# Optimization experiments

Hardware: AMD Instinct MI355X
Metric: run time of the kernel (lower is better)

## Reference

```python
import jax, jax.numpy as jnp
import numpy as np

HEAD_NUM = 16

def setup_inputs() -> dict:
    key = jax.random.key(0)
    k1, k2, k3, k4, k5 = jax.random.split(key, 5)
    B, S, F = 4, 2048, 1024
    return {
        "X": jax.random.normal(k1, (B, S, F), dtype=jnp.float32),
        "residual_score": jax.random.normal(k2, (B, S, F), dtype=jnp.float32),
        "wq": jax.random.normal(k3, (F, F), dtype=jnp.float32) * 0.05,
        "wk": jax.random.normal(k4, (F, F), dtype=jnp.float32) * 0.05,
        "wv": jax.random.normal(k5, (F, F), dtype=jnp.float32) * 0.05,
    }

def reference(X, residual_score, wq, wk, wv):
    B, S, F = X.shape
    H = HEAD_NUM
    D = F // H  # head dim
    # Original scales logits by sqrt(seq_len / head_num), not sqrt(head_dim).
    scale = jnp.sqrt(jnp.asarray(S / H, dtype=X.dtype))
    # QKV projections: [B,S,F] @ [F,F] -> [B,S,F], then split features into heads -> [B,H,S,D]
    def proj(w):
        y = jnp.einsum('bsf,fg->bsg', X, w)
        return y.reshape(B, S, H, D).transpose(0, 2, 1, 3)
    q, k, v = proj(wq), proj(wk), proj(wv)
    logits = jnp.einsum('bhsd,bhtd->bhst', q, k) / scale  # [B,H,S,S]
    attn = jax.nn.softmax(logits, axis=-1)
    effect = jnp.einsum('bhst,bhtd->bhsd', attn, v)  # [B,H,S,D]
    all_effects = effect.transpose(0, 2, 1, 3).reshape(B, S, F)
    out = all_effects + residual_score
    return (out, out)
```

## Files before the change

### kernel.cpp

```cpp
#include <hip/hip_runtime.h>
#include <hip/hip_bf16.h>
#include <stdint.h>

#define B_ 4
#define S_ 2048
#define F_ 1024
#define H_ 16
#define D_ 64
#define M_ (B_*S_)
#define OUTHALF ((size_t)B_*S_*F_)
#define KVB 64
#define QBLK 256

typedef __attribute__((ext_vector_type(4))) float f32x4;
typedef __attribute__((ext_vector_type(8))) short bf16x8;

__device__ __forceinline__ short f2bf(float f) {
  __hip_bfloat16 h = __float2bfloat16(f);
  return *reinterpret_cast<short*>(&h);
}

__device__ __forceinline__ void gl2lds16(const short* g, short* l) {
  __builtin_amdgcn_global_load_lds(
      (const __attribute__((address_space(1))) uint32_t*)g,
      (__attribute__((address_space(3))) uint32_t*)l, 16, 0, 0);
}

#define VMCNT_BAR(N)                                            \
  do {                                                          \
    asm volatile("s_waitcnt vmcnt(" #N ")" ::: "memory");       \
    __builtin_amdgcn_s_barrier();                               \
    asm volatile("" ::: "memory");                              \
  } while (0)

__global__ __launch_bounds__(256) void convert_x(const float* __restrict__ X,
                                                 short* __restrict__ Xb) {
  int i = (blockIdx.x * 256 + threadIdx.x) * 8;
  f32x4 a = *(const f32x4*)(X + i);
  f32x4 b = *(const f32x4*)(X + i + 4);
  bf16x8 o;
  o[0]=f2bf(a[0]); o[1]=f2bf(a[1]); o[2]=f2bf(a[2]); o[3]=f2bf(a[3]);
  o[4]=f2bf(b[0]); o[5]=f2bf(b[1]); o[6]=f2bf(b[2]); o[7]=f2bf(b[3]);
  *(bf16x8*)(Xb + i) = o;
}

__global__ __launch_bounds__(256) void transpose_w(
    const float* __restrict__ wq, const float* __restrict__ wk, const float* __restrict__ wv,
    short* __restrict__ tq, short* __restrict__ tk, short* __restrict__ tv) {
  const float* W = blockIdx.z == 0 ? wq : (blockIdx.z == 1 ? wk : wv);
  short* T = blockIdx.z == 0 ? tq : (blockIdx.z == 1 ? tk : tv);
  __shared__ float tile[32][33];
  int tx = threadIdx.x, ty = threadIdx.y;
  int x = blockIdx.x * 32 + tx;
  int y0 = blockIdx.y * 32;
  #pragma unroll
  for (int j = ty; j < 32; j += 8) tile[j][tx] = W[(size_t)(y0 + j) * F_ + x];
  __syncthreads();
  int x2 = y0 + tx;
  int y2 = blockIdx.x * 32;
  #pragma unroll
  for (int j = ty; j < 32; j += 8) T[(size_t)(y2 + j) * F_ + x2] = f2bf(tile[tx][j]);
}

__global__ __launch_bounds__(256) void gemm_qkv(
    const short* __restrict__ Xb,
    const short* __restrict__ Wtq, const short* __restrict__ Wtk, const short* __restrict__ Wtv,
    short* __restrict__ Qb, short* __restrict__ Kb, short* __restrict__ Vt) {
  __shared__ short As[2][128 * 32];
  __shared__ short Bs[2][128 * 32];
  const int z = blockIdx.z;
  const short* Wt = z == 0 ? Wtq : (z == 1 ? Wtk : Wtv);
  const int m0 = blockIdx.x * 128, n0 = blockIdx.y * 128;
  const int tid = threadIdx.x, wid = tid >> 6, lane = tid & 63;
  const int wm = wid >> 1, wn = wid & 1;
  const int l15 = lane & 15, l4 = lane >> 4;

  f32x4 acc[4][4];
  #pragma unroll
  for (int i = 0; i < 4; ++i)
    #pragma unroll
    for (int j = 0; j < 4; ++j) acc[i][j] = {0.f, 0.f, 0.f, 0.f};

  const int srow = wid * 32 + (lane >> 2);
  const int scol = (lane & 3) * 8;

  auto stage = [&](int buf, int k0) {
    gl2lds16(Xb + (size_t)(m0 + srow) * F_ + k0 + scol,      &As[buf][(wid * 32) * 32]);
    gl2lds16(Xb + (size_t)(m0 + srow + 16) * F_ + k0 + scol, &As[buf][(wid * 32 + 16) * 32]);
    gl2lds16(Wt + (size_t)(n0 + srow) * F_ + k0 + scol,      &Bs[buf][(wid * 32) * 32]);
    gl2lds16(Wt + (size_t)(n0 + srow + 16) * F_ + k0 + scol, &Bs[buf][(wid * 32 + 16) * 32]);
  };

  stage(0, 0);
  const int NT = F_ / 32;
  for (int t = 0; t < NT; ++t) {
    const int buf = t & 1;
    if (t + 1 < NT) {
      stage(buf ^ 1, (t + 1) * 32);
      VMCNT_BAR(4);
    } else {
      VMCNT_BAR(0);
    }
    bf16x8 a[4], b[4];
    #pragma unroll
    for (int mf = 0; mf < 4; ++mf)
      a[mf] = *(const bf16x8*)&As[buf][(wm * 64 + mf * 16 + l15) * 32 + l4 * 8];
    #pragma unroll
    for (int nf = 0; nf < 4; ++nf)
      b[nf] = *(const bf16x8*)&Bs[buf][(wn * 64 + nf * 16 + l15) * 32 + l4 * 8];
    __builtin_amdgcn_s_setprio(1);
    #pragma unroll
    for (int mf = 0; mf < 4; ++mf)
      #pragma unroll
      for (int nf = 0; nf < 4; ++nf)
        acc[mf][nf] = __builtin_amdgcn_mfma_f32_16x16x32_bf16(a[mf], b[nf], acc[mf][nf], 0, 0, 0);
    __builtin_amdgcn_s_setprio(0);
    __builtin_amdgcn_s_barrier();
    asm volatile("" ::: "memory");
  }

  const float qscale = 0.12751784477559752f;
  #pragma unroll
  for (int mf = 0; mf < 4; ++mf)
    #pragma unroll
    for (int nf = 0; nf < 4; ++nf)
      #pragma unroll
      for (int r = 0; r < 4; ++r) {
        float v = acc[mf][nf][r];
        int row = m0 + wm * 64 + mf * 16 + l4 * 4 + r;
        int col = n0 + wn * 64 + nf * 16 + l15;
        int bb = row >> 11, s = row & 2047, h = col >> 6, d = col & 63;
        if (z == 0)
          Qb[((size_t)(bb * H_ + h) * S_ + s) * D_ + d] = f2bf(v * qscale);
        else if (z == 1)
          Kb[((size_t)(bb * H_ + h) * S_ + s) * D_ + d] = f2bf(v);
        else {
          int s5 = s & 31;
          int sp = (s & ~31) | (((s5 >> 2) & 3) << 3) | (((s5 >> 4) & 1) << 2) | (s5 & 3);
          Vt[((size_t)(bb * H_ + h) * D_ + d) * S_ + sp] = f2bf(v);
        }
      }
}

__global__ __launch_bounds__(512, 4) void attn_kernel(
    const short* __restrict__ Qb, const short* __restrict__ Kb, const short* __restrict__ Vt,
    const float* __restrict__ resid, float* __restrict__ out) {
  __shared__ short Ks[2][KVB][64];
  __shared__ short Vs[2][D_][KVB];
  const int bh = blockIdx.y;
  const int b = bh >> 4, h = bh & 15;
  const int qbase = blockIdx.x * QBLK;
  const int wid = threadIdx.x >> 6, lane = threadIdx.x & 63;
  const int l15 = lane & 15, l4 = lane >> 4;
  const short* Qp = Qb + (size_t)bh * S_ * D_;
  const short* Kp = Kb + (size_t)bh * S_ * D_;
  const short* Vp = Vt + (size_t)bh * D_ * S_;

  bf16x8 bq[2][2];
  #pragma unroll
  for (int g = 0; g < 2; ++g) {
    int qr = qbase + wid * 32 + g * 16 + l15;
    bq[g][0] = *(const bf16x8*)&Qp[qr * D_ + l4 * 8];
    bq[g][1] = *(const bf16x8*)&Qp[qr * D_ + 32 + l4 * 8];
  }

  bf16x8 aOnes;
  {
    short onebf = (short)0x3F80;
    #pragma unroll
    for (int i = 0; i < 8; ++i) aOnes[i] = (l15 == 0) ? onebf : (short)0;
  }

  const int sr = wid * 8 + (lane >> 3);
  const int ssrc = ((lane & 7) ^ (lane >> 3)) * 8;

  f32x4 acc[2][4];
  f32x4 accl[2];
  #pragma unroll
  for (int g = 0; g < 2; ++g) {
    accl[g] = {0.f, 0.f, 0.f, 0.f};
    #pragma unroll
    for (int df = 0; df < 4; ++df) acc[g][df] = {0.f, 0.f, 0.f, 0.f};
  }

  gl2lds16(Kp + (0 + sr) * D_ + ssrc, &Ks[0][wid * 8][0]);
  gl2lds16(Vp + (size_t)sr * S_ + 0 + ssrc, &Vs[0][wid * 8][0]);

  const int NT = S_ / KVB;
  for (int t = 0; t < NT; ++t) {
    const int buf = t & 1;
    __syncthreads();
    if (t + 1 < NT) {
      const int kv1 = (t + 1) * KVB;
      gl2lds16(Kp + (kv1 + sr) * D_ + ssrc, &Ks[buf ^ 1][wid * 8][0]);
      gl2lds16(Vp + (size_t)sr * S_ + kv1 + ssrc, &Vs[buf ^ 1][wid * 8][0]);
    }

    f32x4 sf[2][4];
    #pragma unroll
    for (int g = 0; g < 2; ++g)
      #pragma unroll
      for (int nf = 0; nf < 4; ++nf) sf[g][nf] = {0.f, 0.f, 0.f, 0.f};
    __builtin_amdgcn_s_setprio(1);
    #pragma unroll
    for (int nf = 0; nf < 4; ++nf) {
      int row = nf * 16 + l15;
      int c0 = (l4 ^ (row & 7)) * 8;
      int c1 = ((4 + l4) ^ (row & 7)) * 8;
      bf16x8 ak0 = *(const bf16x8*)&Ks[buf][row][c0];
      bf16x8 ak1 = *(const bf16x8*)&Ks[buf][row][c1];
      #pragma unroll
      for (int g = 0; g < 2; ++g) {
        sf[g][nf] = __builtin_amdgcn_mfma_f32_16x16x32_bf16(ak0, bq[g][0], sf[g][nf], 0, 0, 0);
        sf[g][nf] = __builtin_amdgcn_mfma_f32_16x16x32_bf16(ak1, bq[g][1], sf[g][nf], 0, 0, 0);
      }
    }
    __builtin_amdgcn_s_setprio(0);

    bf16x8 pb[2][2];
    #pragma unroll
    for (int g = 0; g < 2; ++g)
      #pragma unroll
      for (int bb = 0; bb < 2; ++bb) {
        bf16x8 p;
        #pragma unroll
        for (int r = 0; r < 4; ++r) {
          p[r]     = f2bf(__builtin_amdgcn_exp2f(sf[g][2 * bb][r]));
          p[4 + r] = f2bf(__builtin_amdgcn_exp2f(sf[g][2 * bb + 1][r]));
        }
        pb[g][bb] = p;
      }

    __builtin_amdgcn_s_setprio(1);
    #pragma unroll
    for (int bb = 0; bb < 2; ++bb) {
      #pragma unroll
      for (int df = 0; df < 4; ++df) {
        int row = df * 16 + l15;
        bf16x8 av = *(const bf16x8*)&Vs[buf][row][((4 * bb + l4) ^ (row & 7)) * 8];
        acc[0][df] = __builtin_amdgcn_mfma_f32_16x16x32_bf16(av, pb[0][bb], acc[0][df], 0, 0, 0);
        acc[1][df] = __builtin_amdgcn_mfma_f32_16x16x32_bf16(av, pb[1][bb], acc[1][df], 0, 0, 0);
      }
      accl[0] = __builtin_amdgcn_mfma_f32_16x16x32_bf16(aOnes, pb[0][bb], accl[0], 0, 0, 0);
      accl[1] = __builtin_amdgcn_mfma_f32_16x16x32_bf16(aOnes, pb[1][bb], accl[1], 0, 0, 0);
    }
    __builtin_amdgcn_s_setprio(0);
  }

  #pragma unroll
  for (int g = 0; g < 2; ++g) {
    float lg = __shfl(accl[g][0], l15);
    float rl = 1.f / lg;
    int s = qbase + wid * 32 + g * 16 + l15;
    #pragma unroll
    for (int df = 0; df < 4; ++df) {
      size_t oi = ((size_t)b * S_ + s) * F_ + h * D_ + df * 16 + l4 * 4;
      f32x4 rv = *(const f32x4*)&resid[oi];
      f32x4 ov;
      #pragma unroll
      for (int r = 0; r < 4; ++r) ov[r] = acc[g][df][r] * rl + rv[r];
      *(f32x4*)&out[oi] = ov;
      *(f32x4*)&out[oi + OUTHALF] = ov;
    }
  }
}

extern "C" void kernel_launch(void* const* d_in, const int* in_sizes, int n_in,
                              void* d_out, int out_size, void* d_ws, size_t ws_size,
                              hipStream_t stream) {
  (void)in_sizes; (void)n_in; (void)out_size; (void)ws_size;
  const float* X     = (const float*)d_in[0];
  const float* resid = (const float*)d_in[1];
  const float* wq    = (const float*)d_in[2];
  const float* wk    = (const float*)d_in[3];
  const float* wv    = (const float*)d_in[4];
  float* out = (float*)d_out;
  char* ws = (char*)d_ws;
  short* Xb  = (short*)(ws);
  short* Wtq = (short*)(ws + (16u << 20));
  short* Wtk = (short*)(ws + (18u << 20));
  short* Wtv = (short*)(ws + (20u << 20));
  short* Qb  = (short*)(ws + (22u << 20));
  short* Kb  = (short*)(ws + (38u << 20));
  short* Vt  = (short*)(ws + (54u << 20));

  convert_x<<<dim3((M_ * F_) / (256 * 8)), 256, 0, stream>>>(X, Xb);
  transpose_w<<<dim3(32, 32, 3), dim3(32, 8), 0, stream>>>(wq, wk, wv, Wtq, Wtk, Wtv);
  gemm_qkv<<<dim3(M_ / 128, F_ / 128, 3), 256, 0, stream>>>(Xb, Wtq, Wtk, Wtv, Qb, Kb, Vt);
  attn_kernel<<<dim3(S_ / QBLK, B_ * H_), 512, 0, stream>>>(Qb, Kb, Vt, resid, out);
}
```

Before: 178.9 us.

## Fuse X fp32-to-bf16 conversion into QKV GEMM and swap attention grid order

```diff
diff --git a/kernel.cpp b/kernel.cpp
--- a/kernel.cpp
+++ b/kernel.cpp
@@ -25,6 +25,11 @@
       (const __attribute__((address_space(1))) uint32_t*)g,
       (__attribute__((address_space(3))) uint32_t*)l, 16, 0, 0);
 }
+__device__ __forceinline__ void gl2lds16f(const float* g, float* l) {
+  __builtin_amdgcn_global_load_lds(
+      (const __attribute__((address_space(1))) uint32_t*)g,
+      (__attribute__((address_space(3))) uint32_t*)l, 16, 0, 0);
+}
 
 #define VMCNT_BAR(N)                                            \
   do {                                                          \
@@ -32,17 +37,6 @@
     __builtin_amdgcn_s_barrier();                               \
     asm volatile("" ::: "memory");                              \
   } while (0)
-
-__global__ __launch_bounds__(256) void convert_x(const float* __restrict__ X,
-                                                 short* __restrict__ Xb) {
-  int i = (blockIdx.x * 256 + threadIdx.x) * 8;
-  f32x4 a = *(const f32x4*)(X + i);
-  f32x4 b = *(const f32x4*)(X + i + 4);
-  bf16x8 o;
-  o[0]=f2bf(a[0]); o[1]=f2bf(a[1]); o[2]=f2bf(a[2]); o[3]=f2bf(a[3]);
-  o[4]=f2bf(b[0]); o[5]=f2bf(b[1]); o[6]=f2bf(b[2]); o[7]=f2bf(b[3]);
-  *(bf16x8*)(Xb + i) = o;
-}
 
 __global__ __launch_bounds__(256) void transpose_w(
     const float* __restrict__ wq, const float* __restrict__ wk, const float* __restrict__ wv,
@@ -63,10 +57,10 @@
 }
 
 __global__ __launch_bounds__(256) void gemm_qkv(
-    const short* __restrict__ Xb,
+    const float* __restrict__ X,
     const short* __restrict__ Wtq, const short* __restrict__ Wtk, const short* __restrict__ Wtv,
     short* __restrict__ Qb, short* __restrict__ Kb, short* __restrict__ Vt) {
-  __shared__ short As[2][128 * 32];
+  __shared__ float As[2][128 * 32];
   __shared__ short Bs[2][128 * 32];
   const int z = blockIdx.z;
   const short* Wt = z == 0 ? Wtq : (z == 1 ? Wtk : Wtv);
@@ -81,14 +75,19 @@
     #pragma unroll
     for (int j = 0; j < 4; ++j) acc[i][j] = {0.f, 0.f, 0.f, 0.f};
 
-  const int srow = wid * 32 + (lane >> 2);
-  const int scol = (lane & 3) * 8;
+  const int arow = lane >> 3;
+  const int acol = ((lane & 7) ^ arow) * 4;
+  const int brow = lane >> 2;
+  const int bcol = (lane & 3) * 8;
 
   auto stage = [&](int buf, int k0) {
-    gl2lds16(Xb + (size_t)(m0 + srow) * F_ + k0 + scol,      &As[buf][(wid * 32) * 32]);
-    gl2lds16(Xb + (size_t)(m0 + srow + 16) * F_ + k0 + scol, &As[buf][(wid * 32 + 16) * 32]);
-    gl2lds16(Wt + (size_t)(n0 + srow) * F_ + k0 + scol,      &Bs[buf][(wid * 32) * 32]);
-    gl2lds16(Wt + (size_t)(n0 + srow + 16) * F_ + k0 + scol, &Bs[buf][(wid * 32 + 16) * 32]);
+    #pragma unroll
+    for (int i = 0; i < 4; ++i) {
+      int rbase = i * 32 + wid * 8;
+      gl2lds16f(X + (size_t)(m0 + rbase + arow) * F_ + k0 + acol, &As[buf][rbase * 32]);
+    }
+    gl2lds16(Wt + (size_t)(n0 + wid * 32 + brow) * F_ + k0 + bcol,      &Bs[buf][(wid * 32) * 32]);
+    gl2lds16(Wt + (size_t)(n0 + wid * 32 + 16 + brow) * F_ + k0 + bcol, &Bs[buf][(wid * 32 + 16) * 32]);
   };
 
   stage(0, 0);
@@ -97,14 +96,22 @@
     const int buf = t & 1;
     if (t + 1 < NT) {
       stage(buf ^ 1, (t + 1) * 32);
-      VMCNT_BAR(4);
+      VMCNT_BAR(6);
     } else {
       VMCNT_BAR(0);
     }
     bf16x8 a[4], b[4];
     #pragma unroll
-    for (int mf = 0; mf < 4; ++mf)
-      a[mf] = *(const bf16x8*)&As[buf][(wm * 64 + mf * 16 + l15) * 32 + l4 * 8];
+    for (int mf = 0; mf < 4; ++mf) {
+      int row = wm * 64 + mf * 16 + l15;
+      int r7 = row & 7;
+      f32x4 lo = *(const f32x4*)&As[buf][row * 32 + (((2 * l4) ^ r7) << 2)];
+      f32x4 hi = *(const f32x4*)&As[buf][row * 32 + (((2 * l4 + 1) ^ r7) << 2)];
+      bf16x8 af;
+      af[0] = f2bf(lo[0]); af[1] = f2bf(lo[1]); af[2] = f2bf(lo[2]); af[3] = f2bf(lo[3]);
+      af[4] = f2bf(hi[0]); af[5] = f2bf(hi[1]); af[6] = f2bf(hi[2]); af[7] = f2bf(hi[3]);
+      a[mf] = af;
+    }
     #pragma unroll
     for (int nf = 0; nf < 4; ++nf)
       b[nf] = *(const bf16x8*)&Bs[buf][(wn * 64 + nf * 16 + l15) * 32 + l4 * 8];
@@ -147,9 +154,9 @@
     const float* __restrict__ resid, float* __restrict__ out) {
   __shared__ short Ks[2][KVB][64];
   __shared__ short Vs[2][D_][KVB];
-  const int bh = blockIdx.y;
+  const int bh = blockIdx.x;
   const int b = bh >> 4, h = bh & 15;
-  const int qbase = blockIdx.x * QBLK;
+  const int qbase = blockIdx.y * QBLK;
   const int wid = threadIdx.x >> 6, lane = threadIdx.x & 63;
   const int l15 = lane & 15, l4 = lane >> 4;
   const short* Qp = Qb + (size_t)bh * S_ * D_;
@@ -276,16 +283,14 @@
   const float* wv    = (const float*)d_in[4];
   float* out = (float*)d_out;
   char* ws = (char*)d_ws;
-  short* Xb  = (short*)(ws);
-  short* Wtq = (short*)(ws + (16u << 20));
-  short* Wtk = (short*)(ws + (18u << 20));
-  short* Wtv = (short*)(ws + (20u << 20));
-  short* Qb  = (short*)(ws + (22u << 20));
-  short* Kb  = (short*)(ws + (38u << 20));
-  short* Vt  = (short*)(ws + (54u << 20));
-
-  convert_x<<<dim3((M_ * F_) / (256 * 8)), 256, 0, stream>>>(X, Xb);
+  short* Wtq = (short*)(ws);
+  short* Wtk = (short*)(ws + (2u << 20));
+  short* Wtv = (short*)(ws + (4u << 20));
+  short* Qb  = (short*)(ws + (6u << 20));
+  short* Kb  = (short*)(ws + (22u << 20));
+  short* Vt  = (short*)(ws + (38u << 20));
+
   transpose_w<<<dim3(32, 32, 3), dim3(32, 8), 0, stream>>>(wq, wk, wv, Wtq, Wtk, Wtv);
-  gemm_qkv<<<dim3(M_ / 128, F_ / 128, 3), 256, 0, stream>>>(Xb, Wtq, Wtk, Wtv, Qb, Kb, Vt);
-  attn_kernel<<<dim3(S_ / QBLK, B_ * H_), 512, 0, stream>>>(Qb, Kb, Vt, resid, out);
-}
+  gemm_qkv<<<dim3(M_ / 128, F_ / 128, 3), 256, 0, stream>>>(X, Wtq, Wtk, Wtv, Qb, Kb, Vt);
+  attn_kernel<<<dim3(B_ * H_, S_ / QBLK), 512, 0, stream>>>(Qb, Kb, Vt, resid, out);
+}
```

New measurement: 196.1 us. 1.1x slower.
